# Kernel optimization log

Measured on AMD Instinct MI355X. Metric: run time of the kernel, lower is better.

## Reference

```python
import jax, jax.numpy as jnp
import numpy as np

N_ATOMS = 50000
IN_DIM = 128
HID = 256
N_ELEM = 4
N_IMG = 500
NNZ = 2_000_000
ELEMENTS = jnp.array([1, 6, 8, 29], dtype=jnp.int64)


def setup_inputs() -> dict:
    key = jax.random.key(0)
    ks = jax.random.split(key, 14)
    fingerprints = jax.random.normal(ks[0], (N_ATOMS, IN_DIM), dtype=jnp.float32)
    # atomic numbers drawn from the supported element set
    elem_idx = jax.random.randint(ks[1], (N_ATOMS,), 0, N_ELEM)
    atomic_numbers = ELEMENTS[elem_idx]
    image_idx = jnp.sort(jax.random.randint(ks[2], (N_ATOMS,), 0, N_IMG))
    # sparse fprimes (COO): [N_ATOMS*IN_DIM, 3*N_ATOMS]
    fprime_rows = jax.random.randint(ks[3], (NNZ,), 0, N_ATOMS * IN_DIM)
    fprime_cols = jax.random.randint(ks[4], (NNZ,), 0, 3 * N_ATOMS)
    fprime_vals = jax.random.normal(ks[5], (NNZ,), dtype=jnp.float32) * 0.1
    # per-element MLP params, stacked over the element axis (torch Linear-style init)
    s0, s1 = 1.0 / np.sqrt(IN_DIM), 1.0 / np.sqrt(HID)
    W0 = jax.random.uniform(ks[6], (N_ELEM, IN_DIM, HID), jnp.float32, -s0, s0)
    b0 = jax.random.uniform(ks[7], (N_ELEM, HID), jnp.float32, -s0, s0)
    W1 = jax.random.uniform(ks[8], (N_ELEM, HID, HID), jnp.float32, -s1, s1)
    b1 = jax.random.uniform(ks[9], (N_ELEM, HID), jnp.float32, -s1, s1)
    W2 = jax.random.uniform(ks[10], (N_ELEM, HID, 1), jnp.float32, -s1, s1)
    b2 = jax.random.uniform(ks[11], (N_ELEM, 1), jnp.float32, -s1, s1)
    return {"fingerprints": fingerprints, "atomic_numbers": atomic_numbers,
            "image_idx": image_idx, "fprime_rows": fprime_rows,
            "fprime_cols": fprime_cols, "fprime_vals": fprime_vals,
            "W0": W0, "b0": b0, "W1": W1, "b1": b1, "W2": W2, "b2": b2}


def _per_atom_energy(fp, atomic_numbers, W0, b0, W1, b1, W2, b2):
    # Run every element-specific MLP over ALL atoms (as the torch module does),
    # then mask by the one-hot element membership and sum over elements.
    h = jnp.tanh(jnp.einsum('nd,edh->enh', fp, W0) + b0[:, None, :])   # [E,N,H]
    h = jnp.tanh(jnp.einsum('enh,ehk->enk', h, W1) + b1[:, None, :])   # [E,N,H]
    out = jnp.einsum('enh,eho->eno', h, W2) + b2[:, None, :]           # [E,N,1]
    mask = (atomic_numbers[None, :] == ELEMENTS[:, None]).astype(fp.dtype)  # [E,N]
    return jnp.sum(mask * out[..., 0], axis=0)                          # [N]


def reference(fingerprints, atomic_numbers, image_idx, fprime_rows,
              fprime_cols, fprime_vals, W0, b0, W1, b1, W2, b2):
    o = _per_atom_energy(fingerprints, atomic_numbers, W0, b0, W1, b1, W2, b2)
    energy = jax.ops.segment_sum(o, image_idx, num_segments=N_IMG)  # [N_IMG]
    # dE/dfp for forces (sum over images == sum over atoms of o)
    g = jax.grad(lambda fp: jnp.sum(
        _per_atom_energy(fp, atomic_numbers, W0, b0, W1, b1, W2, b2)))(fingerprints)
    g_flat = g.reshape(-1)  # [N*D]
    # forces = -fprimes^T @ g_flat, fprimes in COO form
    forces = -jax.ops.segment_sum(fprime_vals * g_flat[fprime_rows],
                                  fprime_cols, num_segments=3 * N_ATOMS)
    return energy, forces.reshape(N_ATOMS, 3)
```

## Files before the change

### kernel.cpp

```cpp
#include <hip/hip_runtime.h>
#include <math.h>

#define N_ATOMS 50000
#define IN_DIM 128
#define HID 256
#define N_ELEM 4
#define N_IMG 500
#define NNZ 2000000

#define CBINS 293
#define CW 512
#define BCAP 8192
#define OCAP 4096
#define PCH 8192
#define NBP ((NNZ + PCH - 1) / PCH)
#define BKB ((N_ATOMS + 255) / 256)

typedef __attribute__((ext_vector_type(8))) short bf16x8;
typedef __attribute__((ext_vector_type(4))) float f32x4;
typedef __attribute__((ext_vector_type(4))) int   i32x4;
typedef __attribute__((ext_vector_type(4))) float fv4;

__device__ __forceinline__ int elem_of(int z) {
    return (z == 1) ? 0 : (z == 6) ? 1 : (z == 8) ? 2 : 3;
}

__device__ __forceinline__ unsigned short f2bf(float f) {
    unsigned u = __float_as_uint(f);
    u += 0x7fffu + ((u >> 16) & 1u);
    return (unsigned short)(u >> 16);
}
__device__ __forceinline__ float bf2f(unsigned short u) {
    return __uint_as_float(((unsigned)u) << 16);
}
__device__ __forceinline__ float tanh_fast(float x) {
    float e = __expf(2.f * x);
    return (e - 1.f) / (e + 1.f);
}

__global__ __launch_bounds__(256) void prep_weights(
    const float* __restrict__ W0, const float* __restrict__ W1,
    unsigned short* __restrict__ W0s1,
    unsigned short* __restrict__ W1s2,
    unsigned short* __restrict__ W1s3,
    unsigned short* __restrict__ W0s4,
    int* __restrict__ counts, int* __restrict__ gcur, int* __restrict__ ocur) {
    if (blockIdx.x == 0) {
        if (threadIdx.x < N_ELEM) counts[threadIdx.x] = 0;
        for (int i = threadIdx.x; i < CBINS; i += 256) gcur[i] = 0;
        if (threadIdx.x == 0) ocur[0] = 0;
    }
    int t = blockIdx.x * 256 + threadIdx.x;
    if (t >= N_ELEM * HID * HID) return;
    int e = t >> 16;
    int rem = t & 65535;
    int k = rem >> 8, n = rem & 255;
    unsigned short w1 = f2bf(W1[t]);
    {
        int lane = (((k >> 3) & 3) << 4) | (n & 15);
        W1s2[(e << 16) + ((((n >> 4) * 8 + (k >> 5)) * 64 + lane) << 3) + (k & 7)] = w1;
    }
    {
        int lane = (((n >> 3) & 3) << 4) | (k & 15);
        W1s3[(e << 16) + ((((k >> 4) * 8 + (n >> 5)) * 64 + lane) << 3) + (n & 7)] = w1;
    }
    if (k < IN_DIM) {
        unsigned short w0 = f2bf(W0[e * (IN_DIM * HID) + rem]);
        {
            int lane = (((k >> 3) & 3) << 4) | (n & 15);
            W0s1[e * (IN_DIM * HID) + ((((n >> 4) * 4 + (k >> 5)) * 64 + lane) << 3) + (k & 7)] = w0;
        }
        {
            int lane = (((n >> 3) & 3) << 4) | (k & 15);
            W0s4[e * (IN_DIM * HID) + ((((k >> 4) * 8 + (n >> 5)) * 64 + lane) << 3) + (n & 7)] = w0;
        }
    }
}

__global__ __launch_bounds__(256) void bucket_and_bin(
    const int* __restrict__ Z, int* __restrict__ counts, int* __restrict__ lists,
    float* __restrict__ F,
    const int* __restrict__ rows, const int* __restrict__ cols,
    const float* __restrict__ vals,
    unsigned* __restrict__ packB, float* __restrict__ valsB,
    int* __restrict__ gcur,
    int* __restrict__ ovfR, int* __restrict__ ovfC, float* __restrict__ ovfV,
    int* __restrict__ ocur) {

    __shared__ int   Lr[PCH];
    __shared__ int   Lc[PCH];
    __shared__ float Lv[PCH];
    __shared__ int   hist[CBINS], pref[CBINS], curs[CBINS], gbase[CBINS];

    const int tid = threadIdx.x;

    if (blockIdx.x >= NBP) {
        int* lcnt = hist;
        int* lbase = pref;
        const int bb = blockIdx.x - NBP;
        for (int idx = bb * 256 + tid; idx < 3 * N_ATOMS; idx += BKB * 256)
            F[idx] = 0.f;
        const int i = bb * 256 + tid;
        if (tid < N_ELEM) lcnt[tid] = 0;
        __syncthreads();
        int e = -1, pos = 0;
        if (i < N_ATOMS) {
            e = elem_of(Z[i]);
            pos = atomicAdd(&lcnt[e], 1);
        }
        __syncthreads();
        if (tid < N_ELEM)
            lbase[tid] = atomicAdd(&counts[tid], lcnt[tid]);
        __syncthreads();
        if (i < N_ATOMS) lists[e * N_ATOMS + lbase[e] + pos] = i;
        return;
    }

    const int base = blockIdx.x * PCH;

    for (int i = tid; i < CBINS; i += 256) hist[i] = 0;
    __syncthreads();

    i32x4 r[8], c[8];
    fv4   v[8];
    int nvalid[8];
#pragma unroll
    for (int j = 0; j < 8; ++j) {
        const int i0 = base + tid * 4 + 1024 * j;
        int nv = NNZ - i0;
        nvalid[j] = nv > 4 ? 4 : (nv < 0 ? 0 : nv);
        if (nvalid[j] == 4) {
            r[j] = __builtin_nontemporal_load((const i32x4*)(rows + i0));
            c[j] = __builtin_nontemporal_load((const i32x4*)(cols + i0));
            v[j] = __builtin_nontemporal_load((const fv4*)(vals + i0));
        } else {
            for (int e2 = 0; e2 < nvalid[j]; ++e2) {
                r[j][e2] = rows[i0 + e2]; c[j][e2] = cols[i0 + e2];
                v[j][e2] = vals[i0 + e2];
            }
        }
#pragma unroll
        for (int e2 = 0; e2 < 4; ++e2)
            if (e2 < nvalid[j]) atomicAdd(&hist[c[j][e2] >> 9], 1);
    }
    __syncthreads();

    if (tid == 0) {
        int s = 0;
        for (int b = 0; b < CBINS; ++b) { pref[b] = s; s += hist[b]; }
    }
    __syncthreads();
    for (int b = tid; b < CBINS; b += 256) {
        gbase[b] = atomicAdd(&gcur[b], hist[b]);
        curs[b] = pref[b];
    }
    __syncthreads();

#pragma unroll
    for (int j = 0; j < 8; ++j)
#pragma unroll
        for (int e2 = 0; e2 < 4; ++e2)
            if (e2 < nvalid[j]) {
                int b = c[j][e2] >> 9;
                int p = atomicAdd(&curs[b], 1);
                Lr[p] = r[j][e2]; Lc[p] = c[j][e2]; Lv[p] = v[j][e2];
            }
    __syncthreads();

    const int total = (base + PCH <= NNZ) ? PCH : (NNZ - base);
#pragma unroll
    for (int j = 0; j < 32; ++j) {
        const int p = tid + 256 * j;
        if (p >= total) break;
        const int col = Lc[p];
        const int b = col >> 9;
        const int g = gbase[b] + (p - pref[b]);
        if (g < BCAP) {
            packB[b * BCAP + g] = ((unsigned)(col & 511) << 23) | (unsigned)Lr[p];
            valsB[b * BCAP + g] = Lv[p];
        } else {
            int od = atomicAdd(ocur, 1);
            if (od < OCAP) { ovfR[od] = Lr[p]; ovfC[od] = col; ovfV[od] = Lv[p]; }
        }
    }
}

#define TILES_PER_E 512
#define CH 1280
__global__ __launch_bounds__(256, 4) void fused_mlp(
    const float* __restrict__ fp,
    const unsigned short* __restrict__ W0s1,
    const unsigned short* __restrict__ W1s2,
    const unsigned short* __restrict__ W1s3,
    const unsigned short* __restrict__ W0s4,
    const float* __restrict__ b0, const float* __restrict__ b1,
    const float* __restrict__ W2, const float* __restrict__ b2,
    float* __restrict__ o_atom,
    unsigned short* __restrict__ Gb,
    const int* __restrict__ counts, const int* __restrict__ lists) {

    const int bid = blockIdx.x;
    const int xcd = bid & 7;
    const int e = xcd & 3;
    const int tile = (bid >> 3) * 2 + (xcd >> 2);
    const int cnt = counts[e];
    const int m0 = tile * 32;
    if (m0 >= cnt) return;
    const int* list = lists + e * N_ATOMS;

    __shared__ short tH[8 * CH];
    __shared__ short tD[8 * CH];

    const int tid = threadIdx.x;
    const int lane = tid & 63;
    const int wv = tid >> 6;
    const int lr = lane & 15;
    const int lq = lane >> 4;

    const unsigned short* B1 = W0s1 + (size_t)e * HID * IN_DIM;
    const unsigned short* B2 = W1s2 + (size_t)e * HID * HID;
    const unsigned short* B3 = W1s3 + (size_t)e * HID * HID;
    const unsigned short* B4 = W0s4 + (size_t)e * IN_DIM * HID;

    f32x4 acc[2][4];
#define ZERO_ACC()                                                        \
    _Pragma("unroll") for (int mt = 0; mt < 2; ++mt)                      \
        _Pragma("unroll") for (int nt = 0; nt < 4; ++nt)                  \
            _Pragma("unroll") for (int j = 0; j < 4; ++j) acc[mt][nt][j] = 0.f;

    {
        bf16x8 bb0[4];
#pragma unroll
        for (int nt = 0; nt < 4; ++nt)
            bb0[nt] = *(const bf16x8*)(B1 +
                ((size_t)(((wv * 4 + nt) * 4 + 0) * 64 + lane) << 3));

#pragma unroll
        for (int p = 0; p < 4; ++p) {
            const int row = p * 8 + (tid >> 5);
            const int col = (tid & 31) * 4;
            const int m = m0 + row;
            float4 a = make_float4(0.f, 0.f, 0.f, 0.f);
            if (m < cnt)
                a = *(const float4*)(fp + (size_t)list[m] * IN_DIM + col);
            short4 b;
            b.x = (short)f2bf(a.x); b.y = (short)f2bf(a.y);
            b.z = (short)f2bf(a.z); b.w = (short)f2bf(a.w);
            *(short4*)&tD[(col >> 5) * CH + row * 40 + (col & 31)] = b;
        }
        __syncthreads();

        ZERO_ACC();
        bf16x8 bb[2][4];
#pragma unroll
        for (int nt = 0; nt < 4; ++nt) bb[0][nt] = bb0[nt];
#pragma unroll
        for (int ki = 0; ki < 4; ++ki) {
            const int cur = ki & 1, nx = cur ^ 1;
            if (ki < 3) {
#pragma unroll
                for (int nt = 0; nt < 4; ++nt)
                    bb[nx][nt] = *(const bf16x8*)(B1 +
                        ((size_t)(((wv * 4 + nt) * 4 + ki + 1) * 64 + lane) << 3));
            }
            bf16x8 af[2];
#pragma unroll
            for (int mt = 0; mt < 2; ++mt)
                af[mt] = *(const bf16x8*)&tD[ki * CH + (mt * 16 + lr) * 40 + lq * 8];
#pragma unroll
            for (int mt = 0; mt < 2; ++mt)
#pragma unroll
                for (int nt = 0; nt < 4; ++nt)
                    acc[mt][nt] = __builtin_amdgcn_mfma_f32_16x16x32_bf16(
                        af[mt], bb[cur][nt], acc[mt][nt], 0, 0, 0);
        }
    }

    bf16x8 b2r[3][4];
#pragma unroll
    for (int p = 0; p < 3; ++p)
#pragma unroll
        for (int nt = 0; nt < 4; ++nt)
            b2r[p][nt] = *(const bf16x8*)(B2 +
                ((size_t)(((wv * 4 + nt) * 8 + p) * 64 + lane) << 3));

    {
        float bv[4];
#pragma unroll
        for (int nt = 0; nt < 4; ++nt)
            bv[nt] = b0[e * HID + wv * 64 + nt * 16 + lr];
#pragma unroll
        for (int mt = 0; mt < 2; ++mt)
#pragma unroll
            for (int rr = 0; rr < 4; ++rr) {
                const int row = mt * 16 + lq * 4 + rr;
#pragma unroll
                for (int nt = 0; nt < 4; ++nt) {
                    const int n = wv * 64 + nt * 16 + lr;
                    float t = tanh_fast(acc[mt][nt][rr] + bv[nt]);
                    tH[(n >> 5) * CH + row * 40 + (n & 31)] = (short)f2bf(t);
                }
            }
    }
    __syncthreads();

    ZERO_ACC();
#pragma unroll
    for (int ki = 0; ki < 8; ++ki) {
        bf16x8 af[2];
#pragma unroll
        for (int mt = 0; mt < 2; ++mt)
            af[mt] = *(const bf16x8*)&tH[ki * CH + (mt * 16 + lr) * 40 + lq * 8];
#pragma unroll
        for (int mt = 0; mt < 2; ++mt)
#pragma unroll
            for (int nt = 0; nt < 4; ++nt)
                acc[mt][nt] = __builtin_amdgcn_mfma_f32_16x16x32_bf16(
                    af[mt], b2r[ki % 3][nt], acc[mt][nt], 0, 0, 0);
        if (ki < 5) {
#pragma unroll
            for (int nt = 0; nt < 4; ++nt)
                b2r[ki % 3][nt] = *(const bf16x8*)(B2 +
                    ((size_t)(((wv * 4 + nt) * 8 + ki + 3) * 64 + lane) << 3));
        }
    }

    bf16x8 b3r[3][4];
#pragma unroll
    for (int p = 0; p < 3; ++p)
#pragma unroll
        for (int nt = 0; nt < 4; ++nt)
            b3r[p][nt] = *(const bf16x8*)(B3 +
                ((size_t)(((wv * 4 + nt) * 8 + p) * 64 + lane) << 3));

    {
        float bv[4], w2v[4];
#pragma unroll
        for (int nt = 0; nt < 4; ++nt) {
            bv[nt]  = b1[e * HID + wv * 64 + nt * 16 + lr];
            w2v[nt] = W2[e * HID + wv * 64 + nt * 16 + lr];
        }
#pragma unroll
        for (int mt = 0; mt < 2; ++mt)
#pragma unroll
            for (int rr = 0; rr < 4; ++rr) {
                const int row = mt * 16 + lq * 4 + rr;
                float osum = 0.f;
#pragma unroll
                for (int nt = 0; nt < 4; ++nt) {
                    const int n = wv * 64 + nt * 16 + lr;
                    float t = tanh_fast(acc[mt][nt][rr] + bv[nt]);
                    osum += t * w2v[nt];
                    tD[(n >> 5) * CH + row * 40 + (n & 31)] =
                        (short)f2bf(w2v[nt] * (1.f - t * t));
                }
                osum += __shfl_xor(osum, 1, 64);
                osum += __shfl_xor(osum, 2, 64);
                osum += __shfl_xor(osum, 4, 64);
                osum += __shfl_xor(osum, 8, 64);
                if (lr == 0)
                    ((float*)&tD[row * 40 + 32])[wv] = osum;
            }
    }
    __syncthreads();
    if (tid < 32) {
        int m = m0 + tid;
        if (m < cnt) {
            const float4 r4 = *(const float4*)&tD[tid * 40 + 32];
            o_atom[list[m]] = r4.x + r4.y + r4.z + r4.w + b2[e];
        }
    }

    ZERO_ACC();
#pragma unroll
    for (int ki = 0; ki < 8; ++ki) {
        bf16x8 af[2];
#pragma unroll
        for (int mt = 0; mt < 2; ++mt)
            af[mt] = *(const bf16x8*)&tD[ki * CH + (mt * 16 + lr) * 40 + lq * 8];
#pragma unroll
        for (int mt = 0; mt < 2; ++mt)
#pragma unroll
            for (int nt = 0; nt < 4; ++nt)
                acc[mt][nt] = __builtin_amdgcn_mfma_f32_16x16x32_bf16(
                    af[mt], b3r[ki % 3][nt], acc[mt][nt], 0, 0, 0);
        if (ki < 5) {
#pragma unroll
            for (int nt = 0; nt < 4; ++nt)
                b3r[ki % 3][nt] = *(const bf16x8*)(B3 +
                    ((size_t)(((wv * 4 + nt) * 8 + ki + 3) * 64 + lane) << 3));
        }
    }

    bf16x8 b4r[3][2];
#pragma unroll
    for (int p = 0; p < 3; ++p)
#pragma unroll
        for (int nt = 0; nt < 2; ++nt)
            b4r[p][nt] = *(const bf16x8*)(B4 +
                ((size_t)(((wv * 2 + nt) * 8 + p) * 64 + lane) << 3));

#pragma unroll
    for (int mt = 0; mt < 2; ++mt)
#pragma unroll
        for (int rr = 0; rr < 4; ++rr) {
            const int row = mt * 16 + lq * 4 + rr;
#pragma unroll
            for (int nt = 0; nt < 4; ++nt) {
                const int n = wv * 64 + nt * 16 + lr;
                const int a = (n >> 5) * CH + row * 40 + (n & 31);
                float h = bf2f((unsigned short)tH[a]);
                tH[a] = (short)f2bf(acc[mt][nt][rr] * (1.f - h * h));
            }
        }
    __syncthreads();

    {
        f32x4 a4[2][2];
#pragma unroll
        for (int mt = 0; mt < 2; ++mt)
#pragma unroll
            for (int nt = 0; nt < 2; ++nt)
#pragma unroll
                for (int j = 0; j < 4; ++j) a4[mt][nt][j] = 0.f;
#pragma unroll
        for (int ki = 0; ki < 8; ++ki) {
            bf16x8 af[2];
#pragma unroll
            for (int mt = 0; mt < 2; ++mt)
                af[mt] = *(const bf16x8*)&tH[ki * CH + (mt * 16 + lr) * 40 + lq * 8];
#pragma unroll
            for (int mt = 0; mt < 2; ++mt)
#pragma unroll
                for (int nt = 0; nt < 2; ++nt)
                    a4[mt][nt] = __builtin_amdgcn_mfma_f32_16x16x32_bf16(
                        af[mt], b4r[ki % 3][nt], a4[mt][nt], 0, 0, 0);
            if (ki < 5) {
#pragma unroll
                for (int nt = 0; nt < 2; ++nt)
                    b4r[ki % 3][nt] = *(const bf16x8*)(B4 +
                        ((size_t)(((wv * 2 + nt) * 8 + ki + 3) * 64 + lane) << 3));
            }
        }
#pragma unroll
        for (int mt = 0; mt < 2; ++mt)
#pragma unroll
            for (int rr = 0; rr < 4; ++rr) {
                const int row = mt * 16 + lq * 4 + rr;
#pragma unroll
                for (int nt = 0; nt < 2; ++nt) {
                    const int n = wv * 32 + nt * 16 + lr;
                    tD[(n >> 5) * CH + row * 40 + (n & 31)] =
                        (short)f2bf(a4[mt][nt][rr]);
                }
            }
    }
    __syncthreads();
#pragma unroll
    for (int t = 0; t < 2; ++t) {
        const int c = tid + 256 * t;
        const int row = c >> 4;
        const int pos = (c & 15) * 8;
        const int m = m0 + row;
        if (m < cnt) {
            bf16x8 v = *(const bf16x8*)&tD[(pos >> 5) * CH + row * 40 + (pos & 31)];
            *(bf16x8*)(Gb + (size_t)list[m] * IN_DIM + pos) = v;
        }
    }
#undef ZERO_ACC
}

__global__ __launch_bounds__(1024) void forces_consumer(
    const unsigned* __restrict__ packB, const float* __restrict__ valsB,
    const int* __restrict__ gcur,
    const unsigned short* __restrict__ g, float* __restrict__ F,
    const float* __restrict__ o_atom, const int* __restrict__ img,
    float* __restrict__ energy,
    const int* __restrict__ ovfR, const int* __restrict__ ovfC,
    const float* __restrict__ ovfV, const int* __restrict__ ocur) {

    const int blk = blockIdx.x;
    __shared__ float win[CW];

    if (blk < CBINS) {
        for (int i = threadIdx.x; i < CW; i += 1024) win[i] = 0.f;
        __syncthreads();
        const int w0 = blk << 9;
        int cnt = gcur[blk]; if (cnt > BCAP) cnt = BCAP;
        const size_t o = (size_t)blk * BCAP;
        for (int idx0 = (int)threadIdx.x * 4; idx0 < cnt; idx0 += 4096) {
            if (idx0 + 4 <= cnt) {
                i32x4 p = *(const i32x4*)((const int*)packB + o + idx0);
                fv4   v = *(const fv4*)(valsB + o + idx0);
                unsigned p0 = (unsigned)p[0], p1 = (unsigned)p[1];
                unsigned p2 = (unsigned)p[2], p3 = (unsigned)p[3];
                float g0 = bf2f(g[p0 & 0x7FFFFFu]), g1 = bf2f(g[p1 & 0x7FFFFFu]);
                float g2 = bf2f(g[p2 & 0x7FFFFFu]), g3 = bf2f(g[p3 & 0x7FFFFFu]);
                atomicAdd(&win[p0 >> 23], -v[0] * g0);
                atomicAdd(&win[p1 >> 23], -v[1] * g1);
                atomicAdd(&win[p2 >> 23], -v[2] * g2);
                atomicAdd(&win[p3 >> 23], -v[3] * g3);
            } else {
                for (int e2 = idx0; e2 < cnt; ++e2) {
                    unsigned p0 = packB[o + e2];
                    atomicAdd(&win[p0 >> 23],
                              -valsB[o + e2] * bf2f(g[p0 & 0x7FFFFFu]));
                }
            }
        }
        int ocnt = ocur[0]; if (ocnt > OCAP) ocnt = OCAP;
        for (int k2 = threadIdx.x; k2 < ocnt; k2 += 1024) {
            int c = ovfC[k2];
            if (c >= w0 && c < w0 + CW)
                atomicAdd(&win[c - w0], -ovfV[k2] * bf2f(g[ovfR[k2]]));
        }
        __syncthreads();
        for (int i = threadIdx.x; i < CW; i += 1024) {
            int c = w0 + i;
            if (c < 3 * N_ATOMS) F[c] = win[i];
        }
    }

    if (blk < N_IMG) {
        const int bb = blk;
        int lo, hi;
        {
            int l = 0, r = N_ATOMS;
            while (l < r) { int m = (l + r) >> 1; if (img[m] < bb) l = m + 1; else r = m; }
            lo = l;
        }
        {
            int l = lo, r = N_ATOMS;
            while (l < r) { int m = (l + r) >> 1; if (img[m] < bb + 1) l = m + 1; else r = m; }
            hi = l;
        }
        float s = 0.f;
        for (int i2 = lo + (int)threadIdx.x; i2 < hi; i2 += 1024) s += o_atom[i2];
#pragma unroll
        for (int off = 32; off > 0; off >>= 1) s += __shfl_down(s, off, 64);
        __shared__ float red[16];
        if ((threadIdx.x & 63) == 0) red[threadIdx.x >> 6] = s;
        __syncthreads();
        if (threadIdx.x == 0) {
            float t = 0.f;
#pragma unroll
            for (int w = 0; w < 16; ++w) t += red[w];
            energy[bb] = t;
        }
    }
}

extern "C" void kernel_launch(void* const* d_in, const int* in_sizes, int n_in,
                              void* d_out, int out_size, void* d_ws, size_t ws_size,
                              hipStream_t stream) {
    const float* fp    = (const float*)d_in[0];
    const int*   Z     = (const int*)d_in[1];
    const int*   img   = (const int*)d_in[2];
    const int*   frows = (const int*)d_in[3];
    const int*   fcols = (const int*)d_in[4];
    const float* fvals = (const float*)d_in[5];
    const float* W0    = (const float*)d_in[6];
    const float* b0    = (const float*)d_in[7];
    const float* W1    = (const float*)d_in[8];
    const float* b1    = (const float*)d_in[9];
    const float* W2    = (const float*)d_in[10];
    const float* b2    = (const float*)d_in[11];

    float* out    = (float*)d_out;
    float* energy = out;
    float* F      = out + N_IMG;

    char* ws = (char*)d_ws;
    int*   counts = (int*)ws;
    int*   lists  = (int*)(ws + 1024);
    char*  base   = ws + (1 << 20);
    unsigned short* Gb   = (unsigned short*)(base);
    float* o_atom        = (float*)(base + 13000000);
    unsigned short* W0s1 = (unsigned short*)(base + 14000000);
    unsigned short* W0s4 = W0s1 + N_ELEM * IN_DIM * HID;
    unsigned short* W1s2 = W0s4 + N_ELEM * IN_DIM * HID;
    unsigned short* W1s3 = W1s2 + N_ELEM * HID * HID;
    int*   gcur  = (int*)(base + 18000000);
    int*   ocur  = (int*)(base + 18002048);
    unsigned* packB = (unsigned*)(base + 19000000);
    float* valsB = (float*)(base + 29000000);
    int*   ovfR  = (int*)(base + 49000000);
    int*   ovfC  = (int*)(base + 49050000);
    float* ovfV  = (float*)(base + 49100000);

    prep_weights<<<(N_ELEM * HID * HID + 255) / 256, 256, 0, stream>>>(
        W0, W1, W0s1, W1s2, W1s3, W0s4, counts, gcur, ocur);

    bucket_and_bin<<<NBP + BKB, 256, 0, stream>>>(
        Z, counts, lists, F, frows, fcols, fvals,
        packB, valsB, gcur, ovfR, ovfC, ovfV, ocur);

    fused_mlp<<<8 * (TILES_PER_E / 2), 256, 0, stream>>>(
        fp, W0s1, W1s2, W1s3, W0s4, b0, b1, W2, b2, o_atom, Gb, counts, lists);

    forces_consumer<<<N_IMG, 1024, 0, stream>>>(
        packB, valsB, gcur, Gb, F, o_atom, img, energy,
        ovfR, ovfC, ovfV, ocur);
}
```

Baseline: 206.9 us.

## Co-schedule COO binning with MLP blocks in one kernel and vectorize weight prep

Moves the sparse-fprime column binning into the same launch as the fused MLP, so binning blocks (now with a smaller chunk size to fit shared memory) overlap with MLP tiles instead of running as a separate serialized pass. The atom bucketing becomes its own small kernel. The weight-swizzle prep is rewritten so each thread produces a packed 8-element bf16 vector write instead of scattered 2-byte stores, with far fewer blocks. The risk is that smaller binning chunks mean more global atomics on the bin cursors, and the shared-memory union may change occupancy.

After: 208.5 us. No clear change (+0.8%).

```diff
diff --git a/kernel.cpp b/kernel.cpp
--- a/kernel.cpp
+++ b/kernel.cpp
@@ -12,7 +12,7 @@
 #define CW 512
 #define BCAP 8192
 #define OCAP 4096
-#define PCH 8192
+#define PCH 2560
 #define NBP ((NNZ + PCH - 1) / PCH)
 #define BKB ((N_ATOMS + 255) / 256)
 
@@ -50,144 +50,84 @@
         for (int i = threadIdx.x; i < CBINS; i += 256) gcur[i] = 0;
         if (threadIdx.x == 0) ocur[0] = 0;
     }
-    int t = blockIdx.x * 256 + threadIdx.x;
-    if (t >= N_ELEM * HID * HID) return;
-    int e = t >> 16;
-    int rem = t & 65535;
-    int k = rem >> 8, n = rem & 255;
-    unsigned short w1 = f2bf(W1[t]);
-    {
-        int lane = (((k >> 3) & 3) << 4) | (n & 15);
-        W1s2[(e << 16) + ((((n >> 4) * 8 + (k >> 5)) * 64 + lane) << 3) + (k & 7)] = w1;
-    }
-    {
-        int lane = (((n >> 3) & 3) << 4) | (k & 15);
-        W1s3[(e << 16) + ((((k >> 4) * 8 + (n >> 5)) * 64 + lane) << 3) + (n & 7)] = w1;
-    }
-    if (k < IN_DIM) {
-        unsigned short w0 = f2bf(W0[e * (IN_DIM * HID) + rem]);
-        {
-            int lane = (((k >> 3) & 3) << 4) | (n & 15);
-            W0s1[e * (IN_DIM * HID) + ((((n >> 4) * 4 + (k >> 5)) * 64 + lane) << 3) + (k & 7)] = w0;
-        }
-        {
-            int lane = (((n >> 3) & 3) << 4) | (k & 15);
-            W0s4[e * (IN_DIM * HID) + ((((k >> 4) * 8 + (n >> 5)) * 64 + lane) << 3) + (n & 7)] = w0;
-        }
-    }
-}
-
-__global__ __launch_bounds__(256) void bucket_and_bin(
-    const int* __restrict__ Z, int* __restrict__ counts, int* __restrict__ lists,
-    float* __restrict__ F,
-    const int* __restrict__ rows, const int* __restrict__ cols,
-    const float* __restrict__ vals,
-    unsigned* __restrict__ packB, float* __restrict__ valsB,
-    int* __restrict__ gcur,
-    int* __restrict__ ovfR, int* __restrict__ ovfC, float* __restrict__ ovfV,
-    int* __restrict__ ocur) {
-
-    __shared__ int   Lr[PCH];
-    __shared__ int   Lc[PCH];
-    __shared__ float Lv[PCH];
-    __shared__ int   hist[CBINS], pref[CBINS], curs[CBINS], gbase[CBINS];
-
+    const int T = blockIdx.x * 256 + threadIdx.x;
+
+    if (T < 32768) {
+        const int e = T >> 13, fid = T & 8191;
+        const int blkv = fid >> 6, lane = fid & 63;
+        const int k0 = ((blkv & 7) << 5) | ((lane >> 4) << 3);
+        const int n  = ((blkv >> 3) << 4) | (lane & 15);
+        const float* src = W1 + e * 65536 + n;
+        bf16x8 vv;
+#pragma unroll
+        for (int j = 0; j < 8; ++j) vv[j] = (short)f2bf(src[(k0 + j) * 256]);
+        *(bf16x8*)(W1s2 + (e << 16) + (fid << 3)) = vv;
+    } else if (T < 65536) {
+        const int u = T - 32768, e = u >> 13, fid = u & 8191;
+        const int blkv = fid >> 6, lane = fid & 63;
+        const int k  = ((blkv >> 3) << 4) | (lane & 15);
+        const int n0 = ((blkv & 7) << 5) | ((lane >> 4) << 3);
+        const float* src = W1 + e * 65536 + k * 256 + n0;
+        float4 a = *(const float4*)src;
+        float4 b = *(const float4*)(src + 4);
+        bf16x8 vv;
+        vv[0] = (short)f2bf(a.x); vv[1] = (short)f2bf(a.y);
+        vv[2] = (short)f2bf(a.z); vv[3] = (short)f2bf(a.w);
+        vv[4] = (short)f2bf(b.x); vv[5] = (short)f2bf(b.y);
+        vv[6] = (short)f2bf(b.z); vv[7] = (short)f2bf(b.w);
+        *(bf16x8*)(W1s3 + (e << 16) + (fid << 3)) = vv;
+    } else if (T < 81920) {
+        const int u = T - 65536, e = u >> 12, fid = u & 4095;
+        const int blkv = fid >> 6, lane = fid & 63;
+        const int k0 = ((blkv & 3) << 5) | ((lane >> 4) << 3);
+        const int n  = ((blkv >> 2) << 4) | (lane & 15);
+        const float* src = W0 + e * 32768 + n;
+        bf16x8 vv;
+#pragma unroll
+        for (int j = 0; j < 8; ++j) vv[j] = (short)f2bf(src[(k0 + j) * 256]);
+        *(bf16x8*)(W0s1 + e * 32768 + (fid << 3)) = vv;
+    } else if (T < 98304) {
+        const int u = T - 81920, e = u >> 12, fid = u & 4095;
+        const int blkv = fid >> 6, lane = fid & 63;
+        const int k  = ((blkv >> 3) << 4) | (lane & 15);
+        const int n0 = ((blkv & 7) << 5) | ((lane >> 4) << 3);
+        const float* src = W0 + e * 32768 + k * 256 + n0;
+        float4 a = *(const float4*)src;
+        float4 b = *(const float4*)(src + 4);
+        bf16x8 vv;
+        vv[0] = (short)f2bf(a.x); vv[1] = (short)f2bf(a.y);
+        vv[2] = (short)f2bf(a.z); vv[3] = (short)f2bf(a.w);
+        vv[4] = (short)f2bf(b.x); vv[5] = (short)f2bf(b.y);
+        vv[6] = (short)f2bf(b.z); vv[7] = (short)f2bf(b.w);
+        *(bf16x8*)(W0s4 + e * 32768 + (fid << 3)) = vv;
+    }
+}
+
+__global__ __launch_bounds__(256) void bucket_atoms(
+    const int* __restrict__ Z, int* __restrict__ counts,
+    int* __restrict__ lists, float* __restrict__ F) {
+    __shared__ int lcnt[N_ELEM], lbase[N_ELEM];
     const int tid = threadIdx.x;
-
-    if (blockIdx.x >= NBP) {
-        int* lcnt = hist;
-        int* lbase = pref;
-        const int bb = blockIdx.x - NBP;
-        for (int idx = bb * 256 + tid; idx < 3 * N_ATOMS; idx += BKB * 256)
-            F[idx] = 0.f;
-        const int i = bb * 256 + tid;
-        if (tid < N_ELEM) lcnt[tid] = 0;
-        __syncthreads();
-        int e = -1, pos = 0;
-        if (i < N_ATOMS) {
-            e = elem_of(Z[i]);
-            pos = atomicAdd(&lcnt[e], 1);
-        }
-        __syncthreads();
-        if (tid < N_ELEM)
-            lbase[tid] = atomicAdd(&counts[tid], lcnt[tid]);
-        __syncthreads();
-        if (i < N_ATOMS) lists[e * N_ATOMS + lbase[e] + pos] = i;
-        return;
-    }
-
-    const int base = blockIdx.x * PCH;
-
-    for (int i = tid; i < CBINS; i += 256) hist[i] = 0;
+    const int bb = blockIdx.x;
+    for (int idx = bb * 256 + tid; idx < 3 * N_ATOMS; idx += BKB * 256)
+        F[idx] = 0.f;
+    const int i = bb * 256 + tid;
+    if (tid < N_ELEM) lcnt[tid] = 0;
     __syncthreads();
-
-    i32x4 r[8], c[8];
-    fv4   v[8];
-    int nvalid[8];
-#pragma unroll
-    for (int j = 0; j < 8; ++j) {
-        const int i0 = base + tid * 4 + 1024 * j;
-        int nv = NNZ - i0;
-        nvalid[j] = nv > 4 ? 4 : (nv < 0 ? 0 : nv);
-        if (nvalid[j] == 4) {
-            r[j] = __builtin_nontemporal_load((const i32x4*)(rows + i0));
-            c[j] = __builtin_nontemporal_load((const i32x4*)(cols + i0));
-            v[j] = __builtin_nontemporal_load((const fv4*)(vals + i0));
-        } else {
-            for (int e2 = 0; e2 < nvalid[j]; ++e2) {
-                r[j][e2] = rows[i0 + e2]; c[j][e2] = cols[i0 + e2];
-                v[j][e2] = vals[i0 + e2];
-            }
-        }
-#pragma unroll
-        for (int e2 = 0; e2 < 4; ++e2)
-            if (e2 < nvalid[j]) atomicAdd(&hist[c[j][e2] >> 9], 1);
+    int e = -1, pos = 0;
+    if (i < N_ATOMS) {
+        e = elem_of(Z[i]);
+        pos = atomicAdd(&lcnt[e], 1);
     }
     __syncthreads();
-
-    if (tid == 0) {
-        int s = 0;
-        for (int b = 0; b < CBINS; ++b) { pref[b] = s; s += hist[b]; }
-    }
+    if (tid < N_ELEM) lbase[tid] = atomicAdd(&counts[tid], lcnt[tid]);
     __syncthreads();
-    for (int b = tid; b < CBINS; b += 256) {
-        gbase[b] = atomicAdd(&gcur[b], hist[b]);
-        curs[b] = pref[b];
-    }
-    __syncthreads();
-
-#pragma unroll
-    for (int j = 0; j < 8; ++j)
-#pragma unroll
-        for (int e2 = 0; e2 < 4; ++e2)
-            if (e2 < nvalid[j]) {
-                int b = c[j][e2] >> 9;
-                int p = atomicAdd(&curs[b], 1);
-                Lr[p] = r[j][e2]; Lc[p] = c[j][e2]; Lv[p] = v[j][e2];
-            }
-    __syncthreads();
-
-    const int total = (base + PCH <= NNZ) ? PCH : (NNZ - base);
-#pragma unroll
-    for (int j = 0; j < 32; ++j) {
-        const int p = tid + 256 * j;
-        if (p >= total) break;
-        const int col = Lc[p];
-        const int b = col >> 9;
-        const int g = gbase[b] + (p - pref[b]);
-        if (g < BCAP) {
-            packB[b * BCAP + g] = ((unsigned)(col & 511) << 23) | (unsigned)Lr[p];
-            valsB[b * BCAP + g] = Lv[p];
-        } else {
-            int od = atomicAdd(ocur, 1);
-            if (od < OCAP) { ovfR[od] = Lr[p]; ovfC[od] = col; ovfV[od] = Lv[p]; }
-        }
-    }
+    if (i < N_ATOMS) lists[e * N_ATOMS + lbase[e] + pos] = i;
 }
 
 #define TILES_PER_E 512
 #define CH 1280
-__global__ __launch_bounds__(256, 4) void fused_mlp(
+__global__ __launch_bounds__(256, 4) void mega_mlp_bin(
     const float* __restrict__ fp,
     const unsigned short* __restrict__ W0s1,
     const unsigned short* __restrict__ W1s2,
@@ -197,21 +137,110 @@
     const float* __restrict__ W2, const float* __restrict__ b2,
     float* __restrict__ o_atom,
     unsigned short* __restrict__ Gb,
-    const int* __restrict__ counts, const int* __restrict__ lists) {
-
+    const int* __restrict__ counts, const int* __restrict__ lists,
+    const int* __restrict__ rows, const int* __restrict__ cols,
+    const float* __restrict__ vals,
+    unsigned* __restrict__ packB, float* __restrict__ valsB,
+    int* __restrict__ gcur,
+    int* __restrict__ ovfR, int* __restrict__ ovfC, float* __restrict__ ovfV,
+    int* __restrict__ ocur) {
+
+    __shared__ __align__(16) char smem[40960];
+    const int tid = threadIdx.x;
     const int bid = blockIdx.x;
-    const int xcd = bid & 7;
+
+    if (bid < NBP) {
+        int*   Lr    = (int*)smem;
+        int*   Lc    = (int*)(smem + 10240);
+        float* Lv    = (float*)(smem + 20480);
+        int*   hist  = (int*)(smem + 30720);
+        int*   pref  = (int*)(smem + 31892);
+        int*   curs  = (int*)(smem + 33064);
+        int*   gbase = (int*)(smem + 34236);
+
+        const int base = bid * PCH;
+        const int lim = (base + PCH <= NNZ) ? PCH : (NNZ - base);
+
+        for (int i = tid; i < CBINS; i += 256) hist[i] = 0;
+        __syncthreads();
+
+        i32x4 r[3], c[3];
+        fv4   v[3];
+        int nvalid[3];
+#pragma unroll
+        for (int j = 0; j < 3; ++j) {
+            const int li = tid * 4 + 1024 * j;
+            const int i0 = base + li;
+            int nv = lim - li;
+            nvalid[j] = nv > 4 ? 4 : (nv < 0 ? 0 : nv);
+            if (nvalid[j] == 4) {
+                r[j] = __builtin_nontemporal_load((const i32x4*)(rows + i0));
+                c[j] = __builtin_nontemporal_load((const i32x4*)(cols + i0));
+                v[j] = __builtin_nontemporal_load((const fv4*)(vals + i0));
+            } else {
+                for (int e2 = 0; e2 < nvalid[j]; ++e2) {
+                    r[j][e2] = rows[i0 + e2]; c[j][e2] = cols[i0 + e2];
+                    v[j][e2] = vals[i0 + e2];
+                }
+            }
+#pragma unroll
+            for (int e2 = 0; e2 < 4; ++e2)
+                if (e2 < nvalid[j]) atomicAdd(&hist[c[j][e2] >> 9], 1);
+        }
+        __syncthreads();
+
+        if (tid == 0) {
+            int s = 0;
+            for (int b = 0; b < CBINS; ++b) { pref[b] = s; s += hist[b]; }
+        }
+        __syncthreads();
+        for (int b = tid; b < CBINS; b += 256) {
+            gbase[b] = atomicAdd(&gcur[b], hist[b]);
+            curs[b] = pref[b];
+        }
+        __syncthreads();
+
+#pragma unroll
+        for (int j = 0; j < 3; ++j)
+#pragma unroll
+            for (int e2 = 0; e2 < 4; ++e2)
+                if (e2 < nvalid[j]) {
+                    int b = c[j][e2] >> 9;
+                    int p = atomicAdd(&curs[b], 1);
+                    Lr[p] = r[j][e2]; Lc[p] = c[j][e2]; Lv[p] = v[j][e2];
+                }
+        __syncthreads();
+
+#pragma unroll
+        for (int j = 0; j < 10; ++j) {
+            const int p = tid + 256 * j;
+            if (p >= lim) break;
+            const int col = Lc[p];
+            const int b = col >> 9;
+            const int g = gbase[b] + (p - pref[b]);
+            if (g < BCAP) {
+                packB[b * BCAP + g] = ((unsigned)(col & 511) << 23) | (unsigned)Lr[p];
+                valsB[b * BCAP + g] = Lv[p];
+            } else {
+                int od = atomicAdd(ocur, 1);
+                if (od < OCAP) { ovfR[od] = Lr[p]; ovfC[od] = col; ovfV[od] = Lv[p]; }
+            }
+        }
+        return;
+    }
+
+    const int fid = bid - NBP;
+    const int xcd = fid & 7;
     const int e = xcd & 3;
-    const int tile = (bid >> 3) * 2 + (xcd >> 2);
+    const int tile = (fid >> 3) * 2 + (xcd >> 2);
     const int cnt = counts[e];
     const int m0 = tile * 32;
     if (m0 >= cnt) return;
     const int* list = lists + e * N_ATOMS;
 
-    __shared__ short tH[8 * CH];
-    __shared__ short tD[8 * CH];
-
-    const int tid = threadIdx.x;
+    short* tH = (short*)smem;
+    short* tD = (short*)(smem + 20480);
+
     const int lane = tid & 63;
     const int wv = tid >> 6;
     const int lr = lane & 15;
@@ -588,15 +617,14 @@
     int*   ovfC  = (int*)(base + 49050000);
     float* ovfV  = (float*)(base + 49100000);
 
-    prep_weights<<<(N_ELEM * HID * HID + 255) / 256, 256, 0, stream>>>(
+    prep_weights<<<384, 256, 0, stream>>>(
         W0, W1, W0s1, W1s2, W1s3, W0s4, counts, gcur, ocur);
 
-    bucket_and_bin<<<NBP + BKB, 256, 0, stream>>>(
-        Z, counts, lists, F, frows, fcols, fvals,
-        packB, valsB, gcur, ovfR, ovfC, ovfV, ocur);
-
-    fused_mlp<<<8 * (TILES_PER_E / 2), 256, 0, stream>>>(
-        fp, W0s1, W1s2, W1s3, W0s4, b0, b1, W2, b2, o_atom, Gb, counts, lists);
+    bucket_atoms<<<BKB, 256, 0, stream>>>(Z, counts, lists, F);
+
+    mega_mlp_bin<<<NBP + 8 * (TILES_PER_E / 2), 256, 0, stream>>>(
+        fp, W0s1, W1s2, W1s3, W0s4, b0, b1, W2, b2, o_atom, Gb, counts, lists,
+        frows, fcols, fvals, packB, valsB, gcur, ovfR, ovfC, ovfV, ocur);
 
     forces_consumer<<<N_IMG, 1024, 0, stream>>>(
         packB, valsB, gcur, Gb, F, o_atom, img, energy,
```
